# Kernel optimization log

Measured on AMD Instinct MI355X. Metric: run time of the kernel, lower is better.

The kernel has to match this reference:

```python
import jax, jax.numpy as jnp
import numpy as np

SOBEL = np.array([[1, 0, -1], [2, 0, -2], [1, 0, -1]], dtype=np.float32)


def _conv3(x, w):
    # 3x3 conv, stride 1, padding 1, no bias (NCHW / OIHW)
    return jax.lax.conv_general_dilated(
        x, w, window_strides=(1, 1), padding='SAME',
        dimension_numbers=('NCHW', 'OIHW', 'NCHW'))


def _sobel_conv(x, wx, wy, w1, b1):
    # |sobel_x| + |sobel_y| followed by 1x1 conv (w1: [O, C])
    e = jnp.abs(_conv3(x, wx)) + jnp.abs(_conv3(x, wy))
    return jnp.einsum('bchw,oc->bohw', e, w1) + b1[None, :, None, None]


def setup_inputs() -> dict:
    key = jax.random.key(0)
    ks = jax.random.split(key, 12)
    B, C, H, W = 2, 64, 64, 64
    dk = C // 8
    sob = jnp.asarray(SOBEL)
    inp = {
        'vi': jax.random.normal(ks[0], (B, C, H, W), jnp.float32),
        'ir': jax.random.normal(ks[1], (B, C, H, W), jnp.float32),
        # Sobel conv weights: torch copy_ broadcasts the 3x3 kernel over [C,C,3,3]
        'wsx_vi': jnp.broadcast_to(sob, (C, C, 3, 3)).copy(),
        'wsy_vi': jnp.broadcast_to(sob.T, (C, C, 3, 3)).copy(),
        'w1_vi': jax.random.normal(ks[2], (dk, C), jnp.float32) * 0.05,
        'b1_vi': jax.random.normal(ks[3], (dk,), jnp.float32) * 0.05,
        'wsx_q': jnp.broadcast_to(sob, (2 * C, 2 * C, 3, 3)).copy(),
        'wsy_q': jnp.broadcast_to(sob.T, (2 * C, 2 * C, 3, 3)).copy(),
        'w1_q': jax.random.normal(ks[4], (dk, 2 * C), jnp.float32) * 0.05,
        'b1_q': jax.random.normal(ks[5], (dk,), jnp.float32) * 0.05,
        'wsx_ir': jnp.broadcast_to(sob, (C, C, 3, 3)).copy(),
        'wsy_ir': jnp.broadcast_to(sob.T, (C, C, 3, 3)).copy(),
        'w1_ir': jax.random.normal(ks[6], (dk, C), jnp.float32) * 0.05,
        'b1_ir': jax.random.normal(ks[7], (dk,), jnp.float32) * 0.05,
        'wv_vi': jax.random.normal(ks[8], (C, C), jnp.float32) * 0.05,
        'bv_vi': jax.random.normal(ks[9], (C,), jnp.float32) * 0.05,
        'wv_ir': jax.random.normal(ks[10], (C, C), jnp.float32) * 0.05,
        'bv_ir': jax.random.normal(ks[11], (C,), jnp.float32) * 0.05,
    }
    return inp


def reference(vi, ir, wsx_vi, wsy_vi, w1_vi, b1_vi, wsx_q, wsy_q, w1_q, b1_q,
              wsx_ir, wsy_ir, w1_ir, b1_ir, wv_vi, bv_vi, wv_ir, bv_ir):
    B, C, H, W = vi.shape
    N = H * W
    # Query from concatenated modalities: [B, N, dk]
    xq = _sobel_conv(jnp.concatenate([vi, ir], axis=1), wsx_q, wsy_q, w1_q, b1_q)
    xq = xq.reshape(B, -1, N).transpose(0, 2, 1)
    # Keys: [B, dk, N]
    vi_xk = _sobel_conv(vi, wsx_vi, wsy_vi, w1_vi, b1_vi).reshape(B, -1, N)
    ir_xk = _sobel_conv(ir, wsx_ir, wsy_ir, w1_ir, b1_ir).reshape(B, -1, N)
    # Values (1x1 convs): [B, C, N]
    vi_xv = (jnp.einsum('bchw,oc->bohw', vi, wv_vi) + bv_vi[None, :, None, None]).reshape(B, C, N)
    ir_xv = (jnp.einsum('bchw,oc->bohw', ir, wv_ir) + bv_ir[None, :, None, None]).reshape(B, C, N)
    # Unscaled attention, softmax over last dim: [B, N, N]
    vi_attn = jax.nn.softmax(jnp.einsum('bnd,bdm->bnm', xq, vi_xk), axis=-1)
    ir_attn = jax.nn.softmax(jnp.einsum('bnd,bdm->bnm', xq, ir_xk), axis=-1)
    # Cross combination: vi value routed by ir attention (and vice versa)
    vi_out = jnp.einsum('bcn,bmn->bcm', vi_xv, ir_attn).reshape(B, C, H, W)
    ir_out = jnp.einsum('bcn,bmn->bcm', ir_xv, vi_attn).reshape(B, C, H, W)
    return vi_out, ir_out
```

## Files before the change

kernel.cpp:

```cpp
#include <hip/hip_runtime.h>
#include <hip/hip_bf16.h>

typedef __attribute__((ext_vector_type(8))) short bf16x8;
typedef __attribute__((ext_vector_type(4))) float f32x4;
typedef __attribute__((ext_vector_type(4))) int   i32x4;


__global__ __launch_bounds__(256) void kP_prep(
    const float* __restrict__ vi, const float* __restrict__ ir,
    const float* __restrict__ wsx_vi, const float* __restrict__ wsy_vi,
    const float* __restrict__ wsx_q,  const float* __restrict__ wsy_q,
    const float* __restrict__ wsx_ir, const float* __restrict__ wsy_ir,
    const float* __restrict__ w1_vi, const float* __restrict__ w1_q,
    const float* __restrict__ b1_q,  const float* __restrict__ w1_ir,
    const float* __restrict__ wv_vi, const float* __restrict__ bv_vi,
    const float* __restrict__ wv_ir, const float* __restrict__ bv_ir,
    float* __restrict__ e, float* __restrict__ scal,
    __hip_bfloat16* __restrict__ Vc) {
    const int t = threadIdx.x;
    if (blockIdx.x < 256) {
        __shared__ __align__(16) char wlds[64 * 128];
        const int bm = blockIdx.x >> 6, nt = blockIdx.x & 63;
        const int b = bm >> 1, mod = bm & 1;
        const float* wv = mod ? wv_ir : wv_vi;
        const float* bv = mod ? bv_ir : bv_vi;
        const float* x = (mod ? ir : vi) + b * (64 * 4096);
        {
            const float* src = wv + t * 16;
            int row = t >> 2, colb = (t & 3) * 32;
            int pk[8];
            #pragma unroll
            for (int j = 0; j < 8; ++j)
                asm("v_cvt_pk_bf16_f32 %0, %1, %2" : "=v"(pk[j])
                    : "v"(src[2 * j]), "v"(src[2 * j + 1]));
            int sw = (row & 7) << 4;
            i32x4 lo = {pk[0], pk[1], pk[2], pk[3]};
            i32x4 hi = {pk[4], pk[5], pk[6], pk[7]};
            *(i32x4*)(wlds + row * 128 + (colb ^ sw)) = lo;
            *(i32x4*)(wlds + row * 128 + ((colb + 16) ^ sw)) = hi;
        }
        __syncthreads();
        const int wvid = t >> 6, lane = t & 63;
        const int col = lane & 15, g = lane >> 4;
        const int n = nt * 64 + wvid * 16 + col;
        bf16x8 afr[4][2];
        #pragma unroll
        for (int cb = 0; cb < 4; ++cb) {
            int row = cb * 16 + col;
            int sw = (row & 7) << 4;
            #pragma unroll
            for (int ks = 0; ks < 2; ++ks)
                afr[cb][ks] = *(const bf16x8*)(wlds + row * 128 + ((ks * 64 + g * 16) ^ sw));
        }
        bf16x8 bfr[2];
        #pragma unroll
        for (int ks = 0; ks < 2; ++ks) {
            const float* xr = x + (ks * 32 + g * 8) * 4096 + n;
            int pk[4];
            #pragma unroll
            for (int j = 0; j < 4; ++j)
                asm("v_cvt_pk_bf16_f32 %0, %1, %2" : "=v"(pk[j])
                    : "v"(xr[(2 * j) * 4096]), "v"(xr[(2 * j + 1) * 4096]));
            i32x4 bi = {pk[0], pk[1], pk[2], pk[3]};
            bfr[ks] = __builtin_bit_cast(bf16x8, bi);
        }
        f32x4 acc[4];
        #pragma unroll
        for (int cb = 0; cb < 4; ++cb)
            #pragma unroll
            for (int r = 0; r < 4; ++r) acc[cb][r] = bv[cb * 16 + g * 4 + r];
        #pragma unroll
        for (int ks = 0; ks < 2; ++ks)
            #pragma unroll
            for (int cb = 0; cb < 4; ++cb)
                acc[cb] = __builtin_amdgcn_mfma_f32_16x16x32_bf16(afr[cb][ks], bfr[ks], acc[cb], 0, 0, 0);
        __hip_bfloat16* outp = Vc + (size_t)(bm * 64) * 4096 + n;
        #pragma unroll
        for (int cb = 0; cb < 4; ++cb)
            #pragma unroll
            for (int r = 0; r < 4; ++r)
                outp[(cb * 16 + g * 4 + r) * 4096] = __float2bfloat16(acc[cb][r]);
    } else {
        __shared__ float sv[256], si[256];
        __shared__ float Ad[8], Cv[8], Ci[8], Bq[8];
        __shared__ float mmred[8];
        const int id = blockIdx.x - 256;
        const int rt = id & 31, b = id >> 5;
        const int r0 = rt * 2;
        const float* xv = vi + b * 64 * 4096;
        const float* xi = ir + b * 64 * 4096;
        if (b == 0 && rt == 0 && t < 8) {
            float a = 0.f;
            for (int c = 0; c < 128; ++c) a += w1_q[t * 128 + c];
            float cv = 0.f, ci = 0.f;
            for (int c = 0; c < 64; ++c) { cv += w1_vi[t * 64 + c]; ci += w1_ir[t * 64 + c]; }
            Ad[t] = a; Cv[t] = cv; Ci[t] = ci; Bq[t] = b1_q[t];
        }
        #pragma unroll
        for (int k = 0; k < 2; ++k) {
            int id2 = t + k * 256;
            int mod = id2 >> 8;
            int entry = id2 & 255;
            int grow = r0 - 1 + (entry >> 6);
            int col = entry & 63;
            float acc = 0.f;
            if (grow >= 0 && grow < 64) {
                const float* x = (mod ? xi : xv) + grow * 64 + col;
                #pragma unroll 16
                for (int c = 0; c < 64; ++c) acc += x[c * 4096];
            }
            (mod ? si : sv)[entry] = acc;
        }
        __syncthreads();
        if (b == 0 && rt == 0 && t == 0) {
            float av = 0, gv = 0, ai = 0, gi = 0;
            for (int d = 0; d < 8; ++d) {
                av += Ad[d] * Cv[d]; gv += Bq[d] * Cv[d];
                ai += Ad[d] * Ci[d]; gi += Bq[d] * Ci[d];
            }
            scal[0] = av; scal[1] = gv; scal[2] = ai; scal[3] = gi;
        }
        if (t < 128) {
            int row = t >> 6, col = t & 63;
            int n = (r0 + row) * 64 + col;
            float nv[3][3], ni[3][3];
            #pragma unroll
            for (int di = 0; di < 3; ++di)
                #pragma unroll
                for (int dj = 0; dj < 3; ++dj) {
                    int cc = col + dj - 1;
                    bool in = (cc >= 0) & (cc < 64);
                    int idx = (row + di) * 64 + (in ? cc : 0);
                    nv[di][dj] = in ? sv[idx] : 0.f;
                    ni[di][dj] = in ? si[idx] : 0.f;
                }
            float gxv = 0, gyv = 0, gxi = 0, gyi = 0, gxq = 0, gyq = 0;
            #pragma unroll
            for (int i = 0; i < 3; ++i)
                #pragma unroll
                for (int j = 0; j < 3; ++j) {
                    int k = i * 3 + j;
                    gxv += nv[i][j] * wsx_vi[k]; gyv += nv[i][j] * wsy_vi[k];
                    gxi += ni[i][j] * wsx_ir[k]; gyi += ni[i][j] * wsy_ir[k];
                    float q = nv[i][j] + ni[i][j];
                    gxq += q * wsx_q[k]; gyq += q * wsy_q[k];
                }
            float ev = fabsf(gxv) + fabsf(gyv);
            float ei = fabsf(gxi) + fabsf(gyi);
            float eq = fabsf(gxq) + fabsf(gyq);
            e[(b * 3 + 0) * 4096 + n] = ev;
            e[(b * 3 + 1) * 4096 + n] = ei;
            e[(b * 3 + 2) * 4096 + n] = eq;
            float mnv = ev, mxv = ev, mni = ei, mxi = ei;
            for (int o = 32; o; o >>= 1) {
                mnv = fminf(mnv, __shfl_down(mnv, o));
                mxv = fmaxf(mxv, __shfl_down(mxv, o));
                mni = fminf(mni, __shfl_down(mni, o));
                mxi = fmaxf(mxi, __shfl_down(mxi, o));
            }
            if ((t & 63) == 0) {
                int w = t >> 6;
                mmred[w * 4 + 0] = mnv; mmred[w * 4 + 1] = mxv;
                mmred[w * 4 + 2] = mni; mmred[w * 4 + 3] = mxi;
            }
        }
        __syncthreads();
        if (t == 0) {
            float* bmn = scal + 16;
            float* bmx = scal + 144;
            bmn[(b * 2 + 0) * 32 + rt] = fminf(mmred[0], mmred[4]);
            bmx[(b * 2 + 0) * 32 + rt] = fmaxf(mmred[1], mmred[5]);
            bmn[(b * 2 + 1) * 32 + rt] = fminf(mmred[2], mmred[6]);
            bmx[(b * 2 + 1) * 32 + rt] = fmaxf(mmred[3], mmred[7]);
        }
    }
}

#define KLEN 1024
#define MT 4
__global__ __launch_bounds__(512, 2) void k4_attn(
        const float* __restrict__ e, const float* __restrict__ scal,
        const __hip_bfloat16* __restrict__ Vc,
        float* __restrict__ Opart, float* __restrict__ Zpart) {
    __shared__ __align__(16) char vbuf[64 * KLEN * 2];
    __shared__ __align__(16) float elds[KLEN];
    const int mt8 = blockIdx.x;
    const int bw  = blockIdx.y;
    const int sp  = blockIdx.z;
    const int b = bw >> 1, which = bw & 1;
    const int amod = which ? 0 : 1;
    const int vmod = which;
    const float* e_att = e + (b * 3 + amod) * 4096;
    const float* e_q   = e + (b * 3 + 2) * 4096;
    const float alpha = scal[which ? 0 : 2];
    const float gamma = scal[which ? 1 : 3];
    const short* Vg = (const short*)(Vc + (size_t)((b * 2 + vmod) * 64) * 4096);

    const int tid = threadIdx.x;
    const int wvw = tid >> 6, lane = tid & 63;
    const int h = wvw >> 2, wvt = wvw & 3;

    float emn = scal[16  + (b * 2 + amod) * 32 + (lane & 31)];
    float emx = scal[144 + (b * 2 + amod) * 32 + (lane & 31)];
    #pragma unroll
    for (int o = 16; o; o >>= 1) {
        emn = fminf(emn, __shfl_xor(emn, o));
        emx = fmaxf(emx, __shfl_xor(emx, o));
    }

    #pragma unroll
    for (int k = 0; k < 16; ++k) {
        int id = tid + k * 512;
        int c = id >> 7, s = id & 127;
        bf16x8 v = *(const bf16x8*)(Vg + c * 4096 + sp * KLEN + s * 8);
        int dst = c * 2048 + ((s * 16) ^ ((c & 31) << 4));
        *(bf16x8*)(vbuf + dst) = v;
    }
    if (tid < 256) {
        f32x4 ev = *(const f32x4*)(e_att + sp * KLEN + tid * 4);
        *(f32x4*)(elds + tid * 4) = ev;
    }
    __syncthreads();

    const int col = lane & 15, g = lane >> 4;
    const float L2E = 1.4426950408889634f;
    float t2[MT], nM2[MT];
    int mbase[MT];
    #pragma unroll
    for (int mt = 0; mt < MT; ++mt) {
        int m = mt8 * 256 + mt * 64 + wvt * 16 + col;
        mbase[mt] = m;
        float t = alpha * e_q[m] + gamma;
        t2[mt]  = t * L2E;
        nM2[mt] = -((t > 0.f) ? t * emx : t * emn) * L2E;
    }

    f32x4 acc[MT][4] = {};
    f32x4 accz[MT] = {};
    bf16x8 ones;
    #pragma unroll
    for (int j = 0; j < 8; ++j) ones[j] = (short)0x3F80;

    for (int it = h * 16; it < h * 16 + 16; ++it) {
        const int n0 = it * 32;
        bf16x8 af[4];
        #pragma unroll
        for (int cb = 0; cb < 4; ++cb) {
            int row = cb * 16 + col;
            int byte = row * 2048 + (((n0 + g * 8) * 2) ^ ((row & 31) << 4));
            af[cb] = *(const bf16x8*)(vbuf + byte);
        }
        f32x4 e0 = *(const f32x4*)(elds + n0 + g * 8);
        f32x4 e1 = *(const f32x4*)(elds + n0 + g * 8 + 4);
        #pragma unroll
        for (int mt = 0; mt < MT; ++mt) {
            float p[8];
            #pragma unroll
            for (int j = 0; j < 4; ++j) {
                float g0 = fmaf(e0[j], t2[mt], nM2[mt]);
                float g1 = fmaf(e1[j], t2[mt], nM2[mt]);
                asm("v_exp_f32 %0, %1" : "=v"(p[j])     : "v"(g0));
                asm("v_exp_f32 %0, %1" : "=v"(p[j + 4]) : "v"(g1));
            }
            int pk0, pk1, pk2, pk3;
            asm("v_cvt_pk_bf16_f32 %0, %1, %2" : "=v"(pk0) : "v"(p[0]), "v"(p[1]));
            asm("v_cvt_pk_bf16_f32 %0, %1, %2" : "=v"(pk1) : "v"(p[2]), "v"(p[3]));
            asm("v_cvt_pk_bf16_f32 %0, %1, %2" : "=v"(pk2) : "v"(p[4]), "v"(p[5]));
            asm("v_cvt_pk_bf16_f32 %0, %1, %2" : "=v"(pk3) : "v"(p[6]), "v"(p[7]));
            i32x4 pki = {pk0, pk1, pk2, pk3};
            bf16x8 bfrag = __builtin_bit_cast(bf16x8, pki);
            #pragma unroll
            for (int cb = 0; cb < 4; ++cb)
                acc[mt][cb] = __builtin_amdgcn_mfma_f32_16x16x32_bf16(af[cb], bfrag, acc[mt][cb], 0, 0, 0);
            accz[mt] = __builtin_amdgcn_mfma_f32_16x16x32_bf16(ones, bfrag, accz[mt], 0, 0, 0);
        }
    }

    __syncthreads();
    float* red = (float*)vbuf;
    if (h == 1) {
        #pragma unroll
        for (int mt = 0; mt < MT; ++mt) {
            int base = ((wvt * 4 + mt) * 64 + lane) * 20;
            #pragma unroll
            for (int cb = 0; cb < 4; ++cb)
                *(f32x4*)(red + base + cb * 4) = acc[mt][cb];
            red[base + 16] = accz[mt][0];
        }
    }
    __syncthreads();
    if (h == 0) {
        float* opb = Opart + (size_t)((bw * 4 + sp) * 64) * 4096;
        #pragma unroll
        for (int mt = 0; mt < MT; ++mt) {
            int base = ((wvt * 4 + mt) * 64 + lane) * 20;
            #pragma unroll
            for (int cb = 0; cb < 4; ++cb)
                acc[mt][cb] += *(const f32x4*)(red + base + cb * 4);
            float z = accz[mt][0] + red[base + 16];
            float* op = opb + mbase[mt];
            #pragma unroll
            for (int cb = 0; cb < 4; ++cb) {
                int c = cb * 16 + g * 4;
                #pragma unroll
                for (int r = 0; r < 4; ++r) op[(c + r) * 4096] = acc[mt][cb][r];
            }
            if (lane < 16) Zpart[(bw * 4 + sp) * 4096 + mbase[mt]] = z;
        }
    }
}

__global__ __launch_bounds__(256) void k5_combine(
        const float* __restrict__ Opart, const float* __restrict__ Zpart,
        float* __restrict__ out) {
    int bw = blockIdx.y; int b = bw >> 1, which = bw & 1;
    int idx = (blockIdx.x * 256 + threadIdx.x) * 4;
    int m = idx & 4095;
    f32x4 num = {}; f32x4 den = {};
    #pragma unroll
    for (int sp = 0; sp < 4; ++sp) {
        num += *(const f32x4*)(Opart + (size_t)((bw * 4 + sp) * 64) * 4096 + idx);
        den += *(const f32x4*)(Zpart + (bw * 4 + sp) * 4096 + m);
    }
    *(f32x4*)(out + which * (2 * 64 * 4096) + b * (64 * 4096) + idx) = num / den;
}

extern "C" void kernel_launch(void* const* d_in, const int* in_sizes, int n_in,
                              void* d_out, int out_size, void* d_ws, size_t ws_size,
                              hipStream_t stream) {
    const float* vi     = (const float*)d_in[0];
    const float* ir     = (const float*)d_in[1];
    const float* wsx_vi = (const float*)d_in[2];
    const float* wsy_vi = (const float*)d_in[3];
    const float* w1_vi  = (const float*)d_in[4];
    const float* wsx_q  = (const float*)d_in[6];
    const float* wsy_q  = (const float*)d_in[7];
    const float* w1_q   = (const float*)d_in[8];
    const float* b1_q   = (const float*)d_in[9];
    const float* wsx_ir = (const float*)d_in[10];
    const float* wsy_ir = (const float*)d_in[11];
    const float* w1_ir  = (const float*)d_in[12];
    const float* wv_vi  = (const float*)d_in[14];
    const float* bv_vi  = (const float*)d_in[15];
    const float* wv_ir  = (const float*)d_in[16];
    const float* bv_ir  = (const float*)d_in[17];
    (void)in_sizes; (void)n_in; (void)out_size;

    char* ws = (char*)d_ws;
    float* scal = (float*)ws;
    float* e    = (float*)(ws + 1280);
    __hip_bfloat16* Vc = (__hip_bfloat16*)(ws + 99584);
    float* Opart = (float*)(ws + 2196736);
    float* Zpart = (float*)(ws + 2196736 + 4ull * 4194304);
    float* out = (float*)d_out;
    (void)ws_size;

    kP_prep<<<dim3(320), 256, 0, stream>>>(vi, ir, wsx_vi, wsy_vi, wsx_q, wsy_q,
                                           wsx_ir, wsy_ir, w1_vi, w1_q, b1_q, w1_ir,
                                           wv_vi, bv_vi, wv_ir, bv_ir, e, scal, Vc);
    k4_attn<<<dim3(16, 4, 4), 512, 0, stream>>>(e, scal, Vc, Opart, Zpart);
    k5_combine<<<dim3(256, 4), 256, 0, stream>>>(Opart, Zpart, out);
}
```

Measured before the change: 37.01 us.

## Remove key split and combine kernel; stream keys through double-buffered LDS

The attention kernel no longer splits the key dimension across four blocks whose partial sums were then reduced by a separate combine kernel. Each block now owns 64 query rows and walks all 4096 keys in 512-wide chunks, double-buffering the V tile and e values in LDS by prefetching the next chunk into registers. It then normalizes by the row sum and writes the output directly. This removes the partial-output round trip through global memory and one kernel launch. In exchange, V is reloaded once per 64 queries rather than once per 256, and each wave does a quarter of the previous work per V fragment load, lowering MFMA reuse.

New measurement: 34.93 us. -5.6%, faster.

```diff
diff --git a/kernel.cpp b/kernel.cpp
--- a/kernel.cpp
+++ b/kernel.cpp
@@ -176,17 +176,16 @@
     }
 }
 
-#define KLEN 1024
-#define MT 4
+#define CH 512
+#define NCH 8
 __global__ __launch_bounds__(512, 2) void k4_attn(
         const float* __restrict__ e, const float* __restrict__ scal,
         const __hip_bfloat16* __restrict__ Vc,
-        float* __restrict__ Opart, float* __restrict__ Zpart) {
-    __shared__ __align__(16) char vbuf[64 * KLEN * 2];
-    __shared__ __align__(16) float elds[KLEN];
-    const int mt8 = blockIdx.x;
-    const int bw  = blockIdx.y;
-    const int sp  = blockIdx.z;
+        float* __restrict__ out) {
+    __shared__ __align__(16) char vbuf[2][64 * CH * 2];
+    __shared__ __align__(16) float elds[2][CH];
+    const int mt = blockIdx.x;
+    const int bw = blockIdx.y;
     const int b = bw >> 1, which = bw & 1;
     const int amod = which ? 0 : 1;
     const int vmod = which;
@@ -199,6 +198,7 @@
     const int tid = threadIdx.x;
     const int wvw = tid >> 6, lane = tid & 63;
     const int h = wvw >> 2, wvt = wvw & 3;
+    const int col = lane & 15, g = lane >> 4;
 
     float emn = scal[16  + (b * 2 + amod) * 32 + (lane & 31)];
     float emx = scal[144 + (b * 2 + amod) * 32 + (lane & 31)];
@@ -208,57 +208,61 @@
         emx = fmaxf(emx, __shfl_xor(emx, o));
     }
 
+    const int m = mt * 64 + wvt * 16 + col;
+    const float L2E = 1.4426950408889634f;
+    const float t  = alpha * e_q[m] + gamma;
+    const float t2 = t * L2E;
+    const float nM2 = -((t > 0.f) ? t * emx : t * emn) * L2E;
+
     #pragma unroll
-    for (int k = 0; k < 16; ++k) {
+    for (int k = 0; k < 8; ++k) {
         int id = tid + k * 512;
-        int c = id >> 7, s = id & 127;
-        bf16x8 v = *(const bf16x8*)(Vg + c * 4096 + sp * KLEN + s * 8);
-        int dst = c * 2048 + ((s * 16) ^ ((c & 31) << 4));
-        *(bf16x8*)(vbuf + dst) = v;
-    }
-    if (tid < 256) {
-        f32x4 ev = *(const f32x4*)(e_att + sp * KLEN + tid * 4);
-        *(f32x4*)(elds + tid * 4) = ev;
-    }
+        int c = id >> 6, s = id & 63;
+        bf16x8 v = *(const bf16x8*)(Vg + c * 4096 + s * 8);
+        *(bf16x8*)(vbuf[0] + c * 1024 + ((s * 16) ^ ((c & 31) << 4))) = v;
+    }
+    elds[0][tid] = e_att[tid];
     __syncthreads();
 
-    const int col = lane & 15, g = lane >> 4;
-    const float L2E = 1.4426950408889634f;
-    float t2[MT], nM2[MT];
-    int mbase[MT];
-    #pragma unroll
-    for (int mt = 0; mt < MT; ++mt) {
-        int m = mt8 * 256 + mt * 64 + wvt * 16 + col;
-        mbase[mt] = m;
-        float t = alpha * e_q[m] + gamma;
-        t2[mt]  = t * L2E;
-        nM2[mt] = -((t > 0.f) ? t * emx : t * emn) * L2E;
-    }
-
-    f32x4 acc[MT][4] = {};
-    f32x4 accz[MT] = {};
+    f32x4 acc[4] = {};
+    f32x4 accz = {};
     bf16x8 ones;
     #pragma unroll
     for (int j = 0; j < 8; ++j) ones[j] = (short)0x3F80;
 
-    for (int it = h * 16; it < h * 16 + 16; ++it) {
-        const int n0 = it * 32;
-        bf16x8 af[4];
-        #pragma unroll
-        for (int cb = 0; cb < 4; ++cb) {
-            int row = cb * 16 + col;
-            int byte = row * 2048 + (((n0 + g * 8) * 2) ^ ((row & 31) << 4));
-            af[cb] = *(const bf16x8*)(vbuf + byte);
-        }
-        f32x4 e0 = *(const f32x4*)(elds + n0 + g * 8);
-        f32x4 e1 = *(const f32x4*)(elds + n0 + g * 8 + 4);
-        #pragma unroll
-        for (int mt = 0; mt < MT; ++mt) {
+    for (int ck = 0; ck < NCH; ++ck) {
+        bf16x8 stg[8];
+        float en = 0.f;
+        const bool pf = (ck + 1 < NCH);
+        if (pf) {
+            const short* src = Vg + (ck + 1) * CH;
+            #pragma unroll
+            for (int k = 0; k < 8; ++k) {
+                int id = tid + k * 512;
+                int c = id >> 6, s = id & 63;
+                stg[k] = *(const bf16x8*)(src + c * 4096 + s * 8);
+            }
+            en = e_att[(ck + 1) * CH + tid];
+        }
+        const char* vb = vbuf[ck & 1];
+        const float* el = elds[ck & 1];
+        #pragma unroll
+        for (int it2 = 0; it2 < 8; ++it2) {
+            const int n0 = (h * 8 + it2) * 32;
+            bf16x8 af[4];
+            #pragma unroll
+            for (int cb = 0; cb < 4; ++cb) {
+                int row = cb * 16 + col;
+                int byte = row * 1024 + (((n0 + g * 8) * 2) ^ ((row & 31) << 4));
+                af[cb] = *(const bf16x8*)(vb + byte);
+            }
+            f32x4 e0 = *(const f32x4*)(el + n0 + g * 8);
+            f32x4 e1 = *(const f32x4*)(el + n0 + g * 8 + 4);
             float p[8];
             #pragma unroll
             for (int j = 0; j < 4; ++j) {
-                float g0 = fmaf(e0[j], t2[mt], nM2[mt]);
-                float g1 = fmaf(e1[j], t2[mt], nM2[mt]);
+                float g0 = fmaf(e0[j], t2, nM2);
+                float g1 = fmaf(e1[j], t2, nM2);
                 asm("v_exp_f32 %0, %1" : "=v"(p[j])     : "v"(g0));
                 asm("v_exp_f32 %0, %1" : "=v"(p[j + 4]) : "v"(g1));
             }
@@ -271,58 +275,47 @@
             bf16x8 bfrag = __builtin_bit_cast(bf16x8, pki);
             #pragma unroll
             for (int cb = 0; cb < 4; ++cb)
-                acc[mt][cb] = __builtin_amdgcn_mfma_f32_16x16x32_bf16(af[cb], bfrag, acc[mt][cb], 0, 0, 0);
-            accz[mt] = __builtin_amdgcn_mfma_f32_16x16x32_bf16(ones, bfrag, accz[mt], 0, 0, 0);
-        }
-    }
-
-    __syncthreads();
-    float* red = (float*)vbuf;
+                acc[cb] = __builtin_amdgcn_mfma_f32_16x16x32_bf16(af[cb], bfrag, acc[cb], 0, 0, 0);
+            accz = __builtin_amdgcn_mfma_f32_16x16x32_bf16(ones, bfrag, accz, 0, 0, 0);
+        }
+        __syncthreads();
+        if (pf) {
+            char* wb = vbuf[(ck + 1) & 1];
+            #pragma unroll
+            for (int k = 0; k < 8; ++k) {
+                int id = tid + k * 512;
+                int c = id >> 6, s = id & 63;
+                *(bf16x8*)(wb + c * 1024 + ((s * 16) ^ ((c & 31) << 4))) = stg[k];
+            }
+            elds[(ck + 1) & 1][tid] = en;
+            __syncthreads();
+        }
+    }
+
+    float* red = (float*)vbuf[0];
     if (h == 1) {
-        #pragma unroll
-        for (int mt = 0; mt < MT; ++mt) {
-            int base = ((wvt * 4 + mt) * 64 + lane) * 20;
-            #pragma unroll
-            for (int cb = 0; cb < 4; ++cb)
-                *(f32x4*)(red + base + cb * 4) = acc[mt][cb];
-            red[base + 16] = accz[mt][0];
-        }
+        int base = (wvt * 64 + lane) * 21;
+        #pragma unroll
+        for (int cb = 0; cb < 4; ++cb)
+            *(f32x4*)(red + base + cb * 4) = acc[cb];
+        red[base + 16] = accz[0];
     }
     __syncthreads();
     if (h == 0) {
-        float* opb = Opart + (size_t)((bw * 4 + sp) * 64) * 4096;
-        #pragma unroll
-        for (int mt = 0; mt < MT; ++mt) {
-            int base = ((wvt * 4 + mt) * 64 + lane) * 20;
-            #pragma unroll
-            for (int cb = 0; cb < 4; ++cb)
-                acc[mt][cb] += *(const f32x4*)(red + base + cb * 4);
-            float z = accz[mt][0] + red[base + 16];
-            float* op = opb + mbase[mt];
-            #pragma unroll
-            for (int cb = 0; cb < 4; ++cb) {
-                int c = cb * 16 + g * 4;
-                #pragma unroll
-                for (int r = 0; r < 4; ++r) op[(c + r) * 4096] = acc[mt][cb][r];
-            }
-            if (lane < 16) Zpart[(bw * 4 + sp) * 4096 + mbase[mt]] = z;
-        }
-    }
-}
-
-__global__ __launch_bounds__(256) void k5_combine(
-        const float* __restrict__ Opart, const float* __restrict__ Zpart,
-        float* __restrict__ out) {
-    int bw = blockIdx.y; int b = bw >> 1, which = bw & 1;
-    int idx = (blockIdx.x * 256 + threadIdx.x) * 4;
-    int m = idx & 4095;
-    f32x4 num = {}; f32x4 den = {};
-    #pragma unroll
-    for (int sp = 0; sp < 4; ++sp) {
-        num += *(const f32x4*)(Opart + (size_t)((bw * 4 + sp) * 64) * 4096 + idx);
-        den += *(const f32x4*)(Zpart + (bw * 4 + sp) * 4096 + m);
-    }
-    *(f32x4*)(out + which * (2 * 64 * 4096) + b * (64 * 4096) + idx) = num / den;
+        int base = (wvt * 64 + lane) * 21;
+        #pragma unroll
+        for (int cb = 0; cb < 4; ++cb)
+            acc[cb] += *(const f32x4*)(red + base + cb * 4);
+        float z = accz[0] + red[base + 16];
+        float inv = 1.0f / z;
+        float* ob = out + which * (2 * 64 * 4096) + b * (64 * 4096) + m;
+        #pragma unroll
+        for (int cb = 0; cb < 4; ++cb) {
+            int c = cb * 16 + g * 4;
+            #pragma unroll
+            for (int r = 0; r < 4; ++r) ob[(c + r) * 4096] = acc[cb][r] * inv;
+        }
+    }
 }
 
 extern "C" void kernel_launch(void* const* d_in, const int* in_sizes, int n_in,
@@ -350,14 +343,11 @@
     float* scal = (float*)ws;
     float* e    = (float*)(ws + 1280);
     __hip_bfloat16* Vc = (__hip_bfloat16*)(ws + 99584);
-    float* Opart = (float*)(ws + 2196736);
-    float* Zpart = (float*)(ws + 2196736 + 4ull * 4194304);
     float* out = (float*)d_out;
     (void)ws_size;
 
     kP_prep<<<dim3(320), 256, 0, stream>>>(vi, ir, wsx_vi, wsy_vi, wsx_q, wsy_q,
                                            wsx_ir, wsy_ir, w1_vi, w1_q, b1_q, w1_ir,
                                            wv_vi, bv_vi, wv_ir, bv_ir, e, scal, Vc);
-    k4_attn<<<dim3(16, 4, 4), 512, 0, stream>>>(e, scal, Vc, Opart, Zpart);
-    k5_combine<<<dim3(256, 4), 256, 0, stream>>>(Opart, Zpart, out);
+    k4_attn<<<dim3(64, 4), 512, 0, stream>>>(e, scal, Vc, out);
 }
```
